# Optimization experiments

Hardware: AMD Instinct MI355X
Metric: run time of the kernel (lower is better)

The kernel has to match this reference:

```python
import jax, jax.numpy as jnp
import numpy as np

B, S, D, H, NE, M = 4, 512, 768, 12, 42, 8
OFFSET = 1  # bert cls offset


def setup_inputs() -> dict:
    key = jax.random.key(0)
    k1, k2, k3, k4 = jax.random.split(key, 4)
    sequence_output = jax.random.normal(k1, (B, S, D), dtype=jnp.float32)
    attention = jax.random.uniform(k2, (B, H, S, S), dtype=jnp.float32)
    mention_pos = jax.random.randint(k3, (B, NE, M), 0, S - 2, dtype=jnp.int32)
    mention_mask = jax.random.randint(k4, (B, NE, M), 0, 2, dtype=jnp.int32)
    mention_mask = mention_mask.at[..., 0].set(1)  # every entity has >=1 mention
    return {"sequence_output": sequence_output, "attention": attention,
            "mention_pos": mention_pos, "mention_mask": mention_mask}


def reference(sequence_output, attention, mention_pos, mention_mask):
    b, s, d = sequence_output.shape
    h = attention.shape[1]
    pos = mention_pos + OFFSET                      # [B,NE,M]
    valid = (mention_mask > 0) & (pos < s)          # start+offset < c check
    pos_c = jnp.clip(pos, 0, s - 1)
    bidx = jnp.arange(b)[:, None, None]

    # ragged gather of mention hidden states / attention rows
    emb_m = sequence_output[bidx, pos_c]            # [B,NE,M,D]
    att_m = attention[bidx, :, pos_c]               # [B,NE,M,H,S]

    # logsumexp pool over valid mentions (zeros if no valid mention)
    masked = jnp.where(valid[..., None], emb_m, -jnp.inf)
    lse = jax.scipy.special.logsumexp(masked, axis=2)          # [B,NE,D]
    has = valid.any(axis=2)
    ent_emb = jnp.where(has[..., None], lse, 0.0)

    # mean pool attention rows over valid mentions
    cnt = jnp.maximum(valid.sum(axis=2), 1).astype(att_m.dtype)
    ent_att = (att_m * valid[..., None, None].astype(att_m.dtype)).sum(axis=2) \
              / cnt[..., None, None]                            # [B,NE,H,S]

    # all-pairs head/tail entity embeddings (index_select over hts pairs)
    hs = jnp.broadcast_to(ent_emb[:, :, None, :], (b, NE, NE, d))
    ts = jnp.broadcast_to(ent_emb[:, None, :, :], (b, NE, NE, d))

    # context-based channel map: pairwise attention fusion
    ht = (ent_att[:, :, None] * ent_att[:, None, :]).mean(axis=3)  # [B,NE,NE,S]
    ht = ht / (ht.sum(axis=-1, keepdims=True) + 1e-5)
    rs = jnp.einsum('bsd,bijs->bijd', sequence_output, ht)         # [B,NE,NE,D]

    return jnp.concatenate([hs, ts, rs], axis=-1)  # [B,NE,NE,3D]
```

## Files before the change

kernel.cpp:

```cpp
#include <hip/hip_runtime.h>
#include <hip/hip_bf16.h>
#include <cfloat>
#include <cmath>

#define B_ 4
#define S_ 512
#define D_ 768
#define H_ 12
#define NE_ 42
#define M_ 8
#define OFFSET_ 1
#define NE2_ (NE_*NE_)
#define OUTC_ (3*D_)
#define HS_ (H_*S_)
#define MPAD_ 1792

typedef __attribute__((ext_vector_type(8))) short short8;
typedef __attribute__((ext_vector_type(4))) float f32x4;

#define GLOAD_LDS16(g, l) __builtin_amdgcn_global_load_lds( \
    (const __attribute__((address_space(1))) unsigned int*)(g), \
    (__attribute__((address_space(3))) unsigned int*)(l), 16, 0, 0)

__global__ void k_prep(const float* __restrict__ seq, __hip_bfloat16* __restrict__ seqT) {
    const int b  = blockIdx.z;
    const int s0 = blockIdx.y * 64;
    const int d0 = blockIdx.x * 64;
    const int t  = threadIdx.x;

    __shared__ float tile[64][65];
#pragma unroll
    for (int i = 0; i < 16; ++i) {
        const int r = (t >> 6) * 16 + i;
        const int c = t & 63;
        tile[r][c] = seq[((size_t)b * S_ + s0 + r) * D_ + d0 + c];
    }
    __syncthreads();
#pragma unroll
    for (int i = 0; i < 16; ++i) {
        const int r = (t >> 6) * 16 + i;
        const int c = t & 63;
        seqT[((size_t)b * D_ + d0 + r) * S_ + s0 + c] = __float2bfloat16(tile[c][r]);
    }
}

__global__ void k_ent_att(const float* __restrict__ att, const int* __restrict__ mpos,
                          const int* __restrict__ mmask, float* __restrict__ ent_att) {
    const int beh = blockIdx.x;
    const int h   = beh % H_;
    const int be  = beh / H_;
    const int b   = be / NE_;

    __shared__ int sp[M_];
    __shared__ int sv[M_];
    if (threadIdx.x < M_) {
        int p  = mpos[be * M_ + threadIdx.x] + OFFSET_;
        int v  = (mmask[be * M_ + threadIdx.x] > 0) && (p < S_);
        int pc = p < 0 ? 0 : (p > S_ - 1 ? S_ - 1 : p);
        sp[threadIdx.x] = pc;
        sv[threadIdx.x] = v;
    }
    __syncthreads();

    int cnt = 0;
#pragma unroll
    for (int m = 0; m < M_; ++m) cnt += sv[m];
    const float inv_cnt = 1.0f / (float)(cnt > 0 ? cnt : 1);

    const float* arow = att + ((size_t)b * H_ + h) * S_ * S_;
    const int s0 = threadIdx.x;
    const int s1 = threadIdx.x + 256;
    float a0 = 0.0f, a1 = 0.0f;
#pragma unroll
    for (int m = 0; m < M_; ++m) {
        if (sv[m]) {
            a0 += arow[(size_t)sp[m] * S_ + s0];
            a1 += arow[(size_t)sp[m] * S_ + s1];
        }
    }
    float* dst = ent_att + ((size_t)be * H_ + h) * S_;
    dst[s0] = a0 * inv_cnt;
    dst[s1] = a1 * inv_cnt;
}

__global__ void k_ent_emb(const float* __restrict__ seq, const int* __restrict__ mpos,
                          const int* __restrict__ mmask, float* __restrict__ ent_emb) {
    const int be = blockIdx.x;
    const int b  = be / NE_;

    __shared__ int sp[M_];
    __shared__ int sv[M_];
    if (threadIdx.x < M_) {
        int p  = mpos[be * M_ + threadIdx.x] + OFFSET_;
        int v  = (mmask[be * M_ + threadIdx.x] > 0) && (p < S_);
        int pc = p < 0 ? 0 : (p > S_ - 1 ? S_ - 1 : p);
        sp[threadIdx.x] = pc;
        sv[threadIdx.x] = v;
    }
    __syncthreads();

    int cnt = 0;
#pragma unroll
    for (int m = 0; m < M_; ++m) cnt += sv[m];
    const bool has = cnt > 0;

    for (int d = threadIdx.x; d < D_; d += blockDim.x) {
        float vals[M_];
        float mx = -FLT_MAX;
#pragma unroll
        for (int m = 0; m < M_; ++m) {
            float v = sv[m] ? seq[((size_t)b * S_ + sp[m]) * D_ + d] : -FLT_MAX;
            vals[m] = v;
            mx = fmaxf(mx, v);
        }
        float o = 0.0f;
        if (has) {
            float ss = 0.0f;
#pragma unroll
            for (int m = 0; m < M_; ++m)
                if (sv[m]) ss += expf(vals[m] - mx);
            o = mx + logf(ss);
        }
        ent_emb[(size_t)be * D_ + d] = o;
    }
}

__global__ void k_ht(const float* __restrict__ ent_att, __hip_bfloat16* __restrict__ htb) {
    const int ij = blockIdx.x;
    const int b  = blockIdx.y;
    const int t  = threadIdx.x;
    __hip_bfloat16* dst = htb + ((size_t)b * MPAD_ + ij) * S_;

    if (ij >= NE2_) {
        __hip_bfloat162 z;
        z.x = __float2bfloat16(0.0f);
        z.y = __float2bfloat16(0.0f);
        *reinterpret_cast<__hip_bfloat162*>(&dst[2 * t]) = z;
        return;
    }
    const int i = ij / NE_;
    const int j = ij - i * NE_;

    const float* Ai = ent_att + ((size_t)b * NE_ + i) * HS_;
    const float* Aj = ent_att + ((size_t)b * NE_ + j) * HS_;

    float v0 = 0.0f, v1 = 0.0f;
#pragma unroll
    for (int h = 0; h < H_; ++h) {
        const float2 a = *reinterpret_cast<const float2*>(&Ai[h * S_ + 2 * t]);
        const float2 c = *reinterpret_cast<const float2*>(&Aj[h * S_ + 2 * t]);
        v0 = fmaf(a.x, c.x, v0);
        v1 = fmaf(a.y, c.y, v1);
    }
    v0 *= (1.0f / H_);
    v1 *= (1.0f / H_);

    float local = v0 + v1;
#pragma unroll
    for (int off = 32; off > 0; off >>= 1) local += __shfl_xor(local, off, 64);
    __shared__ float wsum[4];
    if ((t & 63) == 0) wsum[t >> 6] = local;
    __syncthreads();
    const float inv = 1.0f / (wsum[0] + wsum[1] + wsum[2] + wsum[3] + 1e-5f);

    __hip_bfloat162 r;
    r.x = __float2bfloat16(v0 * inv);
    r.y = __float2bfloat16(v1 * inv);
    *reinterpret_cast<__hip_bfloat162*>(&dst[2 * t]) = r;
}

__global__ void __launch_bounds__(256)
k_gemm(const __hip_bfloat16* __restrict__ htb, const __hip_bfloat16* __restrict__ seqT,
       float* __restrict__ out) {
    const int b     = blockIdx.z;
    const int tileN = blockIdx.x * 64;
    const int tileM = blockIdx.y * 128;
    const int tid   = threadIdx.x;
    const int w     = tid >> 6;
    const int lane  = tid & 63;
    const int wr    = w >> 1;
    const int wc    = w & 1;

    __shared__ unsigned short As[2][128 * 32];
    __shared__ unsigned short Bs[2][64 * 32];

    const __hip_bfloat16* A  = htb  + (size_t)b * MPAD_ * S_;
    const __hip_bfloat16* Bt = seqT + (size_t)b * D_ * S_;

    const int crow = lane >> 2;
    const int ccol = (lane & 3) * 8;

    const int lr = lane & 15;
    const int lk = (lane >> 4) * 8;

    f32x4 acc[4][2];
#pragma unroll
    for (int mf = 0; mf < 4; ++mf)
#pragma unroll
        for (int nf = 0; nf < 2; ++nf) acc[mf][nf] = (f32x4){0.f, 0.f, 0.f, 0.f};

    {
#pragma unroll
        for (int q = 0; q < 2; ++q) {
            const int c = w * 2 + q;
            GLOAD_LDS16(A + (size_t)(tileM + c * 16 + crow) * S_ + ccol, &As[0][c * 512]);
        }
        GLOAD_LDS16(Bt + (size_t)(tileN + w * 16 + crow) * S_ + ccol, &Bs[0][w * 512]);
    }
    __syncthreads();

    for (int it = 0; it < 16; ++it) {
        const int cur = it & 1;
        if (it < 15) {
            const int k0 = (it + 1) * 32;
#pragma unroll
            for (int q = 0; q < 2; ++q) {
                const int c = w * 2 + q;
                GLOAD_LDS16(A + (size_t)(tileM + c * 16 + crow) * S_ + k0 + ccol,
                            &As[cur ^ 1][c * 512]);
            }
            GLOAD_LDS16(Bt + (size_t)(tileN + w * 16 + crow) * S_ + k0 + ccol,
                        &Bs[cur ^ 1][w * 512]);
        }

        short8 af[4], bfr[2];
#pragma unroll
        for (int mf = 0; mf < 4; ++mf)
            af[mf] = *(const short8*)&As[cur][(wr * 64 + mf * 16 + lr) * 32 + lk];
#pragma unroll
        for (int nf = 0; nf < 2; ++nf)
            bfr[nf] = *(const short8*)&Bs[cur][(wc * 32 + nf * 16 + lr) * 32 + lk];
#pragma unroll
        for (int mf = 0; mf < 4; ++mf)
#pragma unroll
            for (int nf = 0; nf < 2; ++nf)
                acc[mf][nf] = __builtin_amdgcn_mfma_f32_16x16x32_bf16(af[mf], bfr[nf], acc[mf][nf], 0, 0, 0);

        __syncthreads();
    }

#pragma unroll
    for (int mf = 0; mf < 4; ++mf) {
        const int row0 = tileM + wr * 64 + mf * 16 + (lane >> 4) * 4;
#pragma unroll
        for (int nf = 0; nf < 2; ++nf) {
            const int col = tileN + wc * 32 + nf * 16 + (lane & 15);
#pragma unroll
            for (int j = 0; j < 4; ++j) {
                const int r = row0 + j;
                if (r < NE2_)
                    out[((size_t)(b * NE2_ + r)) * OUTC_ + 2 * D_ + col] = acc[mf][nf][j];
            }
        }
    }
}

__global__ void k_hsts(const float* __restrict__ ent_emb, float* __restrict__ out) {
    const int bij = blockIdx.x;
    const int b   = bij / NE2_;
    const int ij  = bij - b * NE2_;
    const int i   = ij / NE_;
    const int j   = ij - i * NE_;

    const float4* ei = reinterpret_cast<const float4*>(ent_emb + ((size_t)b * NE_ + i) * D_);
    const float4* ej = reinterpret_cast<const float4*>(ent_emb + ((size_t)b * NE_ + j) * D_);
    float4* o = reinterpret_cast<float4*>(out + (size_t)bij * OUTC_);

    for (int t = threadIdx.x; t < D_ / 4; t += blockDim.x) o[t] = ei[t];
    for (int t = threadIdx.x; t < D_ / 4; t += blockDim.x) o[D_ / 4 + t] = ej[t];
}

extern "C" void kernel_launch(void* const* d_in, const int* in_sizes, int n_in,
                              void* d_out, int out_size, void* d_ws, size_t ws_size,
                              hipStream_t stream) {
    const float* seq   = (const float*)d_in[0];
    const float* att   = (const float*)d_in[1];
    const int*   mpos  = (const int*)d_in[2];
    const int*   mmask = (const int*)d_in[3];
    float* out = (float*)d_out;

    float* ent_emb = (float*)d_ws;
    float* ent_att = ent_emb + (size_t)B_ * NE_ * D_;
    __hip_bfloat16* htb  = (__hip_bfloat16*)(ent_att + (size_t)B_ * NE_ * HS_);
    __hip_bfloat16* seqT = htb + (size_t)B_ * MPAD_ * S_;

    k_prep<<<dim3(D_ / 64, S_ / 64, B_), 256, 0, stream>>>(seq, seqT);
    k_ent_att<<<B_ * NE_ * H_, 256, 0, stream>>>(att, mpos, mmask, ent_att);
    k_ent_emb<<<B_ * NE_, 256, 0, stream>>>(seq, mpos, mmask, ent_emb);
    k_ht<<<dim3(MPAD_, B_), 256, 0, stream>>>(ent_att, htb);
    k_gemm<<<dim3(D_ / 64, MPAD_ / 128, B_), 256, 0, stream>>>(htb, seqT, out);
    k_hsts<<<B_ * NE2_, 256, 0, stream>>>(ent_emb, out);
}
```

Baseline: 157.0 us.

## Exploit symmetry of pairwise attention map to compute only upper-triangle pairs

The pairwise attention product ht[i,j] is symmetric in i and j, so only the 903 upper-triangle pairs are computed in k_ht and fed to the GEMM. The GEMM's M dimension drops from 1792 to 1024 padded rows, and each result row is written to both (i,j) and (j,i) in the output. This roughly halves the ht construction and GEMM work. In exchange it adds triangular index inversion via sqrt in the epilogue and produces scattered duplicate stores.

```diff
diff --git a/kernel.cpp b/kernel.cpp
--- a/kernel.cpp
+++ b/kernel.cpp
@@ -13,7 +13,8 @@
 #define NE2_ (NE_*NE_)
 #define OUTC_ (3*D_)
 #define HS_ (H_*S_)
-#define MPAD_ 1792
+#define NU_ 903
+#define MU_ 1024
 
 typedef __attribute__((ext_vector_type(8))) short short8;
 typedef __attribute__((ext_vector_type(4))) float f32x4;
@@ -21,6 +22,16 @@
 #define GLOAD_LDS16(g, l) __builtin_amdgcn_global_load_lds( \
     (const __attribute__((address_space(1))) unsigned int*)(g), \
     (__attribute__((address_space(3))) unsigned int*)(l), 16, 0, 0)
+
+__device__ __forceinline__ int tri_base(int i) { return (i * (2 * NE_ + 1 - i)) >> 1; }
+__device__ __forceinline__ void tri_inv(int r, int& i, int& j) {
+    i = (int)floorf(((float)(2 * NE_ + 1)
+                     - sqrtf((float)((2 * NE_ + 1) * (2 * NE_ + 1)) - 8.0f * (float)r)) * 0.5f);
+    if (i < 0) i = 0;
+    while (tri_base(i + 1) <= r) ++i;
+    while (tri_base(i) > r) --i;
+    j = i + (r - tri_base(i));
+}
 
 __global__ void k_prep(const float* __restrict__ seq, __hip_bfloat16* __restrict__ seqT) {
     const int b  = blockIdx.z;
@@ -126,20 +137,20 @@
 }
 
 __global__ void k_ht(const float* __restrict__ ent_att, __hip_bfloat16* __restrict__ htb) {
-    const int ij = blockIdx.x;
-    const int b  = blockIdx.y;
-    const int t  = threadIdx.x;
-    __hip_bfloat16* dst = htb + ((size_t)b * MPAD_ + ij) * S_;
-
-    if (ij >= NE2_) {
+    const int r = blockIdx.x;
+    const int b = blockIdx.y;
+    const int t = threadIdx.x;
+    __hip_bfloat16* dst = htb + ((size_t)b * MU_ + r) * S_;
+
+    if (r >= NU_) {
         __hip_bfloat162 z;
         z.x = __float2bfloat16(0.0f);
         z.y = __float2bfloat16(0.0f);
         *reinterpret_cast<__hip_bfloat162*>(&dst[2 * t]) = z;
         return;
     }
-    const int i = ij / NE_;
-    const int j = ij - i * NE_;
+    int i, j;
+    tri_inv(r, i, j);
 
     const float* Ai = ent_att + ((size_t)b * NE_ + i) * HS_;
     const float* Aj = ent_att + ((size_t)b * NE_ + j) * HS_;
@@ -163,10 +174,10 @@
     __syncthreads();
     const float inv = 1.0f / (wsum[0] + wsum[1] + wsum[2] + wsum[3] + 1e-5f);
 
-    __hip_bfloat162 r;
-    r.x = __float2bfloat16(v0 * inv);
-    r.y = __float2bfloat16(v1 * inv);
-    *reinterpret_cast<__hip_bfloat162*>(&dst[2 * t]) = r;
+    __hip_bfloat162 rr;
+    rr.x = __float2bfloat16(v0 * inv);
+    rr.y = __float2bfloat16(v1 * inv);
+    *reinterpret_cast<__hip_bfloat162*>(&dst[2 * t]) = rr;
 }
 
 __global__ void __launch_bounds__(256)
@@ -184,7 +195,7 @@
     __shared__ unsigned short As[2][128 * 32];
     __shared__ unsigned short Bs[2][64 * 32];
 
-    const __hip_bfloat16* A  = htb  + (size_t)b * MPAD_ * S_;
+    const __hip_bfloat16* A  = htb  + (size_t)b * MU_ * S_;
     const __hip_bfloat16* Bt = seqT + (size_t)b * D_ * S_;
 
     const int crow = lane >> 2;
@@ -246,10 +257,16 @@
         for (int nf = 0; nf < 2; ++nf) {
             const int col = tileN + wc * 32 + nf * 16 + (lane & 15);
 #pragma unroll
-            for (int j = 0; j < 4; ++j) {
-                const int r = row0 + j;
-                if (r < NE2_)
-                    out[((size_t)(b * NE2_ + r)) * OUTC_ + 2 * D_ + col] = acc[mf][nf][j];
+            for (int jj = 0; jj < 4; ++jj) {
+                const int r = row0 + jj;
+                if (r < NU_) {
+                    int pi, pj;
+                    tri_inv(r, pi, pj);
+                    const float v = acc[mf][nf][jj];
+                    out[((size_t)(b * NE2_ + pi * NE_ + pj)) * OUTC_ + 2 * D_ + col] = v;
+                    if (pi != pj)
+                        out[((size_t)(b * NE2_ + pj * NE_ + pi)) * OUTC_ + 2 * D_ + col] = v;
+                }
             }
         }
     }
@@ -282,12 +299,12 @@
     float* ent_emb = (float*)d_ws;
     float* ent_att = ent_emb + (size_t)B_ * NE_ * D_;
     __hip_bfloat16* htb  = (__hip_bfloat16*)(ent_att + (size_t)B_ * NE_ * HS_);
-    __hip_bfloat16* seqT = htb + (size_t)B_ * MPAD_ * S_;
+    __hip_bfloat16* seqT = htb + (size_t)B_ * MU_ * S_;
 
     k_prep<<<dim3(D_ / 64, S_ / 64, B_), 256, 0, stream>>>(seq, seqT);
     k_ent_att<<<B_ * NE_ * H_, 256, 0, stream>>>(att, mpos, mmask, ent_att);
     k_ent_emb<<<B_ * NE_, 256, 0, stream>>>(seq, mpos, mmask, ent_emb);
-    k_ht<<<dim3(MPAD_, B_), 256, 0, stream>>>(ent_att, htb);
-    k_gemm<<<dim3(D_ / 64, MPAD_ / 128, B_), 256, 0, stream>>>(htb, seqT, out);
+    k_ht<<<dim3(MU_, B_), 256, 0, stream>>>(ent_att, htb);
+    k_gemm<<<dim3(D_ / 64, MU_ / 128, B_), 256, 0, stream>>>(htb, seqT, out);
     k_hsts<<<B_ * NE2_, 256, 0, stream>>>(ent_emb, out);
 }
```

After: 151.4 us. 1.04x faster.
